# Performance work log

Measured on AMD Instinct MI355X. Metric: run time of the kernel, lower is better.

Reference implementation:

```python
import jax, jax.numpy as jnp
import numpy as np

N = 5_000_000   # total nodes
B = 16384       # number of graphs
F_X = 4
F_U = 1


def setup_inputs() -> dict:
    key = jax.random.key(0)
    k = jax.random.split(key, 6)
    x = jax.random.normal(k[0], (N, F_X), dtype=jnp.float32)
    batch = jnp.sort(jax.random.randint(k[1], (N,), 0, B)).astype(jnp.int64)
    u = jax.random.normal(k[2], (B, F_U), dtype=jnp.float32)
    d = F_U + F_X  # 5
    W1 = jax.random.normal(k[3], (d, d), dtype=jnp.float32) / np.sqrt(d)
    b1 = jnp.zeros((d,), dtype=jnp.float32)
    W2 = jax.random.normal(k[4], (d, F_U), dtype=jnp.float32) / np.sqrt(d)
    b2 = jnp.zeros((F_U,), dtype=jnp.float32)
    return {"x": x, "batch": batch, "u": u, "W1": W1, "b1": b1, "W2": W2, "b2": b2}


def reference(x, batch, u, W1, b1, W2, b2):
    # scatter_mean(x, batch, dim=0): segment sum / segment count (empty -> 0)
    seg_sum = jax.ops.segment_sum(x, batch, num_segments=B)            # [B, F_x]
    cnt = jax.ops.segment_sum(jnp.ones((x.shape[0],), x.dtype), batch,
                              num_segments=B)                          # [B]
    mean = jnp.where(cnt[:, None] > 0, seg_sum / jnp.maximum(cnt, 1.0)[:, None], 0.0)
    h = jnp.concatenate([u, mean], axis=1)                             # [B, 5]
    h = jax.nn.leaky_relu(h @ W1 + b1, negative_slope=0.1)
    return h @ W2 + b2                                                 # [B, 1]
```

## Files before the change

### kernel.cpp

```cpp
#include <hip/hip_runtime.h>

#define WAVE 64

__global__ void find_starts4_kernel(const int* __restrict__ batch,
                                    int* __restrict__ seg_start,
                                    int N, int B) {
    const int tid  = blockIdx.x * blockDim.x + threadIdx.x;
    const int lane = threadIdx.x & (WAVE - 1);
    const long long i0 = (long long)tid * 4;
    const bool in   = (i0 < N);
    const bool full = (i0 + 3 < N);

    int4 q = make_int4(0, 0, 0, 0);
    if (full) q = ((const int4*)batch)[tid];

    int prevw = __shfl_up(q.w, 1);

    if (!in) return;

    int prev;
    if (lane == 0) prev = (i0 == 0) ? -1 : batch[i0 - 1];
    else           prev = prevw;

    if (full) {
        int e[4] = {q.x, q.y, q.z, q.w};
        #pragma unroll
        for (int k = 0; k < 4; ++k) {
            int cur = e[k];
            for (int s = prev + 1; s <= cur; ++s) seg_start[s] = (int)(i0 + k);
            prev = cur;
        }
    } else {
        for (long long j = i0; j < N; ++j) {
            int cur = batch[j];
            for (int s = prev + 1; s <= cur; ++s) seg_start[s] = (int)j;
            prev = cur;
        }
    }

    if (i0 + 4 >= N) {
        for (int s = prev + 1; s <= B; ++s) seg_start[s] = N;
    }
}

__global__ void __launch_bounds__(256)
seg_mean_mlp_kernel(const float4* __restrict__ x,
                    const int* __restrict__ seg_start,
                    const float* __restrict__ u,
                    const float* __restrict__ W1,
                    const float* __restrict__ b1,
                    const float* __restrict__ W2,
                    const float* __restrict__ b2,
                    float* __restrict__ out, int B) {
    const int wid  = (blockIdx.x * blockDim.x + threadIdx.x) / WAVE;
    const int lane = threadIdx.x & (WAVE - 1);
    if (wid >= B) return;

    const int start = seg_start[wid];
    const int end   = seg_start[wid + 1];

    float4 a0 = make_float4(0.f, 0.f, 0.f, 0.f);
    float4 a1 = make_float4(0.f, 0.f, 0.f, 0.f);

    int i = start + lane;
    for (; i + WAVE < end; i += 2 * WAVE) {
        float4 v0 = x[i];
        float4 v1 = x[i + WAVE];
        a0.x += v0.x; a0.y += v0.y; a0.z += v0.z; a0.w += v0.w;
        a1.x += v1.x; a1.y += v1.y; a1.z += v1.z; a1.w += v1.w;
    }
    if (i < end) {
        float4 v = x[i];
        a0.x += v.x; a0.y += v.y; a0.z += v.z; a0.w += v.w;
    }
    a0.x += a1.x; a0.y += a1.y; a0.z += a1.z; a0.w += a1.w;

    #pragma unroll
    for (int off = 32; off > 0; off >>= 1) {
        a0.x += __shfl_down(a0.x, off);
        a0.y += __shfl_down(a0.y, off);
        a0.z += __shfl_down(a0.z, off);
        a0.w += __shfl_down(a0.w, off);
    }

    if (lane == 0) {
        const int cnt = end - start;
        const float inv = (cnt > 0) ? (1.0f / (float)cnt) : 0.0f;

        float h[5];
        h[0] = u[wid];
        h[1] = a0.x * inv;
        h[2] = a0.y * inv;
        h[3] = a0.z * inv;
        h[4] = a0.w * inv;

        float o = b2[0];
        #pragma unroll
        for (int j = 0; j < 5; ++j) {
            float s = b1[j];
            #pragma unroll
            for (int i2 = 0; i2 < 5; ++i2) s += h[i2] * W1[i2 * 5 + j];
            s = (s > 0.0f) ? s : 0.1f * s;
            o += s * W2[j];
        }
        out[wid] = o;
    }
}

extern "C" void kernel_launch(void* const* d_in, const int* in_sizes, int n_in,
                              void* d_out, int out_size, void* d_ws, size_t ws_size,
                              hipStream_t stream) {
    const float* x     = (const float*)d_in[0];
    const int*   batch = (const int*)  d_in[1];
    const float* u     = (const float*)d_in[2];
    const float* W1    = (const float*)d_in[3];
    const float* b1    = (const float*)d_in[4];
    const float* W2    = (const float*)d_in[5];
    const float* b2    = (const float*)d_in[6];
    float* out = (float*)d_out;

    const int N = in_sizes[0] / 4;
    const int B = out_size;

    int* seg_start = (int*)d_ws;

    const int quads = (N + 3) / 4;
    find_starts4_kernel<<<(quads + 255) / 256, 256, 0, stream>>>(batch, seg_start, N, B);

    const int threads = 256;
    const int blocks  = (int)(((long long)B * WAVE + threads - 1) / threads);
    seg_mean_mlp_kernel<<<blocks, threads, 0, stream>>>(
        (const float4*)x, seg_start, u, W1, b1, W2, b2, out, B);
}
```

Measured before the change: 144.5 us.

## Replace segment-start kernel with per-wave binary search and unroll accumulation 4x

Drops the separate pass that scans the whole sorted batch array to build segment offsets. Each wave now finds its segment bounds with a binary search over batch, with lanes 0 and 1 searching for the start and end in parallel. The reduction loop is also unrolled to four independent float4 accumulators. This removes one kernel launch and a full read of the batch array, at the cost of about 23 dependent, mostly uncached loads per wave before the reduction can begin.

After: 149.3 us. +3.3%, slower.

```diff
diff --git a/kernel.cpp b/kernel.cpp
--- a/kernel.cpp
+++ b/kernel.cpp
@@ -2,78 +2,54 @@
 
 #define WAVE 64
 
-__global__ void find_starts4_kernel(const int* __restrict__ batch,
-                                    int* __restrict__ seg_start,
-                                    int N, int B) {
-    const int tid  = blockIdx.x * blockDim.x + threadIdx.x;
-    const int lane = threadIdx.x & (WAVE - 1);
-    const long long i0 = (long long)tid * 4;
-    const bool in   = (i0 < N);
-    const bool full = (i0 + 3 < N);
-
-    int4 q = make_int4(0, 0, 0, 0);
-    if (full) q = ((const int4*)batch)[tid];
-
-    int prevw = __shfl_up(q.w, 1);
-
-    if (!in) return;
-
-    int prev;
-    if (lane == 0) prev = (i0 == 0) ? -1 : batch[i0 - 1];
-    else           prev = prevw;
-
-    if (full) {
-        int e[4] = {q.x, q.y, q.z, q.w};
-        #pragma unroll
-        for (int k = 0; k < 4; ++k) {
-            int cur = e[k];
-            for (int s = prev + 1; s <= cur; ++s) seg_start[s] = (int)(i0 + k);
-            prev = cur;
-        }
-    } else {
-        for (long long j = i0; j < N; ++j) {
-            int cur = batch[j];
-            for (int s = prev + 1; s <= cur; ++s) seg_start[s] = (int)j;
-            prev = cur;
-        }
-    }
-
-    if (i0 + 4 >= N) {
-        for (int s = prev + 1; s <= B; ++s) seg_start[s] = N;
-    }
-}
-
 __global__ void __launch_bounds__(256)
-seg_mean_mlp_kernel(const float4* __restrict__ x,
-                    const int* __restrict__ seg_start,
-                    const float* __restrict__ u,
-                    const float* __restrict__ W1,
-                    const float* __restrict__ b1,
-                    const float* __restrict__ W2,
-                    const float* __restrict__ b2,
-                    float* __restrict__ out, int B) {
-    const int wid  = (blockIdx.x * blockDim.x + threadIdx.x) / WAVE;
+fused_seg_mean_mlp(const float4* __restrict__ x,
+                   const int* __restrict__ batch,
+                   const float* __restrict__ u,
+                   const float* __restrict__ W1,
+                   const float* __restrict__ b1,
+                   const float* __restrict__ W2,
+                   const float* __restrict__ b2,
+                   float* __restrict__ out,
+                   int N, int B) {
+    const int wid  = (blockIdx.x * blockDim.x + threadIdx.x) >> 6;
     const int lane = threadIdx.x & (WAVE - 1);
     if (wid >= B) return;
 
-    const int start = seg_start[wid];
-    const int end   = seg_start[wid + 1];
+    const int t = wid + (lane & 1);
+    int lo = 0, hi = N;
+    while (lo < hi) {
+        const int mid = (lo + hi) >> 1;
+        if (batch[mid] < t) lo = mid + 1;
+        else                hi = mid;
+    }
+    const int start = __shfl(lo, 0);
+    const int end   = __shfl(lo, 1);
 
     float4 a0 = make_float4(0.f, 0.f, 0.f, 0.f);
     float4 a1 = make_float4(0.f, 0.f, 0.f, 0.f);
+    float4 a2 = make_float4(0.f, 0.f, 0.f, 0.f);
+    float4 a3 = make_float4(0.f, 0.f, 0.f, 0.f);
 
     int i = start + lane;
-    for (; i + WAVE < end; i += 2 * WAVE) {
+    for (; i + 3 * WAVE < end; i += 4 * WAVE) {
         float4 v0 = x[i];
         float4 v1 = x[i + WAVE];
+        float4 v2 = x[i + 2 * WAVE];
+        float4 v3 = x[i + 3 * WAVE];
         a0.x += v0.x; a0.y += v0.y; a0.z += v0.z; a0.w += v0.w;
         a1.x += v1.x; a1.y += v1.y; a1.z += v1.z; a1.w += v1.w;
+        a2.x += v2.x; a2.y += v2.y; a2.z += v2.z; a2.w += v2.w;
+        a3.x += v3.x; a3.y += v3.y; a3.z += v3.z; a3.w += v3.w;
     }
-    if (i < end) {
+    for (; i < end; i += WAVE) {
         float4 v = x[i];
         a0.x += v.x; a0.y += v.y; a0.z += v.z; a0.w += v.w;
     }
+
     a0.x += a1.x; a0.y += a1.y; a0.z += a1.z; a0.w += a1.w;
+    a2.x += a3.x; a2.y += a3.y; a2.z += a3.z; a2.w += a3.w;
+    a0.x += a2.x; a0.y += a2.y; a0.z += a2.z; a0.w += a2.w;
 
     #pragma unroll
     for (int off = 32; off > 0; off >>= 1) {
@@ -122,13 +98,10 @@
     const int N = in_sizes[0] / 4;
     const int B = out_size;
 
-    int* seg_start = (int*)d_ws;
-
-    const int quads = (N + 3) / 4;
-    find_starts4_kernel<<<(quads + 255) / 256, 256, 0, stream>>>(batch, seg_start, N, B);
+    (void)d_ws; (void)ws_size;
 
     const int threads = 256;
     const int blocks  = (int)(((long long)B * WAVE + threads - 1) / threads);
-    seg_mean_mlp_kernel<<<blocks, threads, 0, stream>>>(
-        (const float4*)x, seg_start, u, W1, b1, W2, b2, out, B);
+    fused_seg_mean_mlp<<<blocks, threads, 0, stream>>>(
+        (const float4*)x, batch, u, W1, b1, W2, b2, out, N, B);
 }
```
